# Performance work log

Measured on AMD Instinct MI355X. Metric: run time of the kernel, lower is better.

Reference implementation:

```python
import jax, jax.numpy as jnp
import numpy as np

B, NA, NT, P, DA, DM, H = 1, 4096, 1024, 32768, 128, 512, 4
DH = DA // H
DF = 4 * DA
WINDOW = 16


def _layer_norm(x, g=None, b=None, eps=1e-5):
    m = jnp.mean(x, axis=-1, keepdims=True)
    v = jnp.var(x, axis=-1, keepdims=True)
    xn = (x - m) / jnp.sqrt(v + eps)
    if g is not None:
        xn = xn * g + b
    return xn


def setup_inputs() -> dict:
    key = jax.random.key(0)
    ks = jax.random.split(key, 32)
    r = lambda k, s: (jax.random.normal(k, s, dtype=jnp.float32) * 0.05)
    return {
        'q': r(ks[0], (B, NA, DA)),
        'c_atom': r(ks[1], (B, NA, DA)),
        'h_cond': r(ks[2], (B, NT, DM)),
        'p_lm': r(ks[3], (B, P, 16)),
        't_emb': r(ks[4], (B, DA)),
        'cond_proj_w': r(ks[5], (DM, DA)), 'cond_proj_b': r(ks[6], (DA,)),
        'adaln1_w': r(ks[7], (DA, 2 * DA)), 'adaln1_b': r(ks[8], (2 * DA,)),
        'adaln2_w': r(ks[9], (DA, 2 * DA)), 'adaln2_b': r(ks[10], (2 * DA,)),
        'ln_g': jnp.ones((DA,), jnp.float32), 'ln_b': jnp.zeros((DA,), jnp.float32),
        'wq': r(ks[11], (DA, DA)), 'wk': r(ks[12], (DA, DA)),
        'wv': r(ks[13], (DA, DA)), 'wg': r(ks[14], (DA, DA)),
        'wo': r(ks[15], (DA, DA)),
        'pair_w': r(ks[16], (16, H)), 'pair_b': r(ks[17], (H,)),
        'gate1_w': r(ks[18], (DA, DA)), 'gate1_b': r(ks[19], (DA,)),
        'gate2_w': r(ks[20], (DA, DA)), 'gate2_b': r(ks[21], (DA,)),
        'sw1': r(ks[22], (DA, DF)), 'sw3': r(ks[23], (DA, DF)),
        'sw2': r(ks[24], (DF, DA)),
        'p_lm_idx': jax.random.randint(ks[25], (B, P, 2), 0, NA, dtype=jnp.int32),
        'token_idx': jnp.sort(jax.random.randint(ks[26], (B, NA), 0, NT, dtype=jnp.int32), axis=-1),
    }


def _forward(q, c_atom, h_cond, p_lm, t_emb,
             cond_proj_w, cond_proj_b, adaln1_w, adaln1_b, adaln2_w, adaln2_b,
             ln_g, ln_b, wq, wk, wv, wg, wo, pair_w, pair_b,
             gate1_w, gate1_b, gate2_w, gate2_b, sw1, sw3, sw2,
             p_lm_idx, token_idx):
    Bq, N, D = q.shape
    # gather token conditioning to atoms: (B, NA, DM)
    h_atoms = jax.vmap(lambda h, t: h[t])(h_cond, token_idx)
    cond = t_emb[:, None, :] + h_atoms @ cond_proj_w + cond_proj_b  # (B, NA, DA)
    g1, b1 = jnp.split(cond @ adaln1_w + adaln1_b, 2, axis=-1)
    q_n = (1.0 + g1) * _layer_norm(q, ln_g, ln_b) + b1

    Q = (q_n @ wq).reshape(Bq, N, H, DH)
    K = (q_n @ wk).reshape(Bq, N, H, DH)
    V = (q_n @ wv).reshape(Bq, N, H, DH)
    G_flat = q_n @ wg  # (B, N, DA); permute/reshape in torch is identity on layout

    scores = jnp.einsum('bihd,bjhd->bhij', Q, K) / jnp.sqrt(jnp.float32(DH))

    # scattered pair bias: (B, P, H) -> dense (B, H, N, N)
    bias = p_lm @ pair_w + pair_b  # (B, P, H)

    def scat(idx, bb):
        return jnp.zeros((N, N, H), bb.dtype).at[idx[:, 0], idx[:, 1]].set(bb)

    pair_bias = jax.vmap(scat)(p_lm_idx, bias).transpose(0, 3, 1, 2)
    scores = scores + pair_bias

    pos = jnp.arange(N)
    window = jnp.abs(pos[:, None] - pos[None, :]) <= WINDOW  # (N, N)
    scores = jnp.where(window[None, None, :, :], scores, -jnp.inf)

    attn = jax.nn.softmax(scores, axis=-1)
    att_out = jnp.einsum('bhij,bjhd->bihd', attn, V).reshape(Bq, N, D)

    q1 = q + jax.nn.sigmoid(G_flat) * (att_out @ wo)
    q1 = q1 + jax.nn.sigmoid(c_atom @ gate1_w + gate1_b) * q1

    g2, b2 = jnp.split(cond @ adaln2_w + adaln2_b, 2, axis=-1)
    q_n2 = (1.0 + g2) * _layer_norm(q1) + b2
    swi = (jax.nn.silu(q_n2 @ sw1) * (q_n2 @ sw3)) @ sw2
    q2 = q1 + jax.nn.sigmoid(c_atom @ gate2_w + gate2_b) * swi
    return q2  # atom_pad_mask is all-ones -> final mask multiply is identity


def reference(q, c_atom, h_cond, p_lm, t_emb,
              cond_proj_w, cond_proj_b, adaln1_w, adaln1_b, adaln2_w, adaln2_b,
              ln_g, ln_b, wq, wk, wv, wg, wo, pair_w, pair_b,
              gate1_w, gate1_b, gate2_w, gate2_b, sw1, sw3, sw2,
              p_lm_idx, token_idx):
    return _forward(q, c_atom, h_cond, p_lm, t_emb,
                    cond_proj_w, cond_proj_b, adaln1_w, adaln1_b, adaln2_w, adaln2_b,
                    ln_g, ln_b, wq, wk, wv, wg, wo, pair_w, pair_b,
                    gate1_w, gate1_b, gate2_w, gate2_b, sw1, sw3, sw2,
                    p_lm_idx, token_idx)
```

## Files before the change

### kernel.cpp

```cpp
#include <hip/hip_runtime.h>
#include <math.h>

#define NA   4096
#define DA   128
#define DM   512
#define NT   1024
#define HH   4
#define DF   512
#define PP   32768
#define WIN  16
#define BAND 33

typedef __attribute__((ext_vector_type(8))) short bf16x8;
typedef __attribute__((ext_vector_type(4))) float f32x4;

__device__ __forceinline__ float sigmoidf_(float x) { return 1.0f / (1.0f + __expf(-x)); }
__device__ __forceinline__ ushort f2bf(float f) {
    union { float f; unsigned int i; } x; x.f = f;
    unsigned int r = x.i + 0x7fffu + ((x.i >> 16) & 1u);
    return (ushort)(r >> 16);
}

__global__ __launch_bounds__(256) void k_prep(
    const float* __restrict__ hc, const float* __restrict__ ca,
    const float* __restrict__ cw, const float* __restrict__ a1, const float* __restrict__ a2,
    const float* __restrict__ wq, const float* __restrict__ wk, const float* __restrict__ wv,
    const float* __restrict__ wg, const float* __restrict__ wo,
    const float* __restrict__ g1, const float* __restrict__ g2,
    const float* __restrict__ s1, const float* __restrict__ s3, const float* __restrict__ s2,
    ushort* hcb, ushort* cab, ushort* cwT, ushort* a1T, ushort* a2T,
    ushort* wqT, ushort* wkT, ushort* wvT, ushort* wgT, ushort* woT,
    ushort* g1T, ushort* g2T, ushort* s1T, ushort* s3T, ushort* s2T)
{
    const float* src; ushort* dst; int logK = 0, N = 0, total = 0, tr = 1;
    switch (blockIdx.y) {
        case 0:  src = hc; dst = hcb; total = NT * DM; tr = 0; break;
        case 1:  src = ca; dst = cab; total = NA * DA; tr = 0; break;
        case 2:  src = cw; dst = cwT; logK = 9; N = 128; break;
        case 3:  src = a1; dst = a1T; logK = 7; N = 256; break;
        case 4:  src = a2; dst = a2T; logK = 7; N = 256; break;
        case 5:  src = wq; dst = wqT; logK = 7; N = 128; break;
        case 6:  src = wk; dst = wkT; logK = 7; N = 128; break;
        case 7:  src = wv; dst = wvT; logK = 7; N = 128; break;
        case 8:  src = wg; dst = wgT; logK = 7; N = 128; break;
        case 9:  src = wo; dst = woT; logK = 7; N = 128; break;
        case 10: src = g1; dst = g1T; logK = 7; N = 128; break;
        case 11: src = g2; dst = g2T; logK = 7; N = 128; break;
        case 12: src = s1; dst = s1T; logK = 7; N = 512; break;
        case 13: src = s3; dst = s3T; logK = 7; N = 512; break;
        default: src = s2; dst = s2T; logK = 9; N = 128; break;
    }
    if (tr) total = N << logK;
    for (int e = blockIdx.x * 256 + threadIdx.x; e < total; e += 64 * 256) {
        float v;
        if (tr) {
            int n = e >> logK, k = e & ((1 << logK) - 1);
            v = src[(size_t)k * N + n];
        } else {
            v = src[e];
        }
        dst[e] = f2bf(v);
    }
}

__global__ __launch_bounds__(256) void k_scatter(
    const float* __restrict__ p_lm, const float* __restrict__ pair_w,
    const float* __restrict__ pair_b, const int* __restrict__ idx,
    float* __restrict__ band)
{
    int p = blockIdx.x * 256 + threadIdx.x;
    if (p >= PP) return;
    int i = idx[2 * p], j = idx[2 * p + 1];
    int d = j - i + WIN;
    if (d < 0 || d > 2 * WIN) return;
    float v0 = pair_b[0], v1 = pair_b[1], v2 = pair_b[2], v3 = pair_b[3];
    #pragma unroll
    for (int k = 0; k < 16; ++k) {
        float a = p_lm[p * 16 + k];
        v0 = fmaf(a, pair_w[k * 4 + 0], v0);
        v1 = fmaf(a, pair_w[k * 4 + 1], v1);
        v2 = fmaf(a, pair_w[k * 4 + 2], v2);
        v3 = fmaf(a, pair_w[k * 4 + 3], v3);
    }
    size_t base = ((size_t)i * HH) * BAND + d;
    band[base + 0 * BAND] = v0;
    band[base + 1 * BAND] = v1;
    band[base + 2 * BAND] = v2;
    band[base + 3 * BAND] = v3;
}

template<int K, int NF>
__device__ __forceinline__ void gemm_core(
    const ushort* __restrict__ Arow, const ushort* __restrict__ WTcol,
    f32x4* acc, int ko)
{
    #pragma unroll
    for (int ks = 0; ks < K / 32; ++ks) {
        bf16x8 a = *(const bf16x8*)(Arow + ks * 32 + ko);
        #pragma unroll
        for (int nf = 0; nf < NF; ++nf) {
            bf16x8 b = *(const bf16x8*)(WTcol + (size_t)nf * 16 * K + ks * 32 + ko);
            acc[nf] = __builtin_amdgcn_mfma_f32_16x16x32_bf16(a, b, acc[nf], 0, 0, 0);
        }
    }
}

__global__ __launch_bounds__(256) void k_cond(
    const ushort* __restrict__ hcb, const int* __restrict__ tok,
    const ushort* __restrict__ cwT, const float* __restrict__ t_emb,
    const float* __restrict__ cond_b, ushort* __restrict__ cond_bf)
{
    const int tid = threadIdx.x, l = tid & 63, w = tid >> 6;
    const int cl = l & 15, ko = (l >> 4) * 8;
    const int m0 = blockIdx.x * 64, n0 = blockIdx.y * 32;
    const int trow = tok[m0 + w * 16 + cl];
    f32x4 acc[2] = {};
    gemm_core<512, 2>(hcb + (size_t)trow * DM, cwT + (size_t)(n0 + cl) * DM, acc, ko);
    const int r0 = m0 + w * 16 + (l >> 4) * 4;
    #pragma unroll
    for (int nf = 0; nf < 2; ++nf) {
        int col = n0 + nf * 16 + cl;
        float add = t_emb[col] + cond_b[col];
        #pragma unroll
        for (int r = 0; r < 4; ++r)
            cond_bf[(size_t)(r0 + r) * DA + col] = f2bf(acc[nf][r] + add);
    }
}

__global__ __launch_bounds__(256) void k_ada(
    const ushort* __restrict__ cond_bf,
    const ushort* __restrict__ a1T, const ushort* __restrict__ a2T,
    const float* __restrict__ b1, const float* __restrict__ b2,
    float* __restrict__ gb1, float* __restrict__ gb2)
{
    const int tid = threadIdx.x, l = tid & 63, w = tid >> 6;
    const int cl = l & 15, ko = (l >> 4) * 8;
    const int m0 = blockIdx.x * 64, n0 = blockIdx.y * 64;
    const ushort* WT = blockIdx.z ? a2T : a1T;
    const float* bias = blockIdx.z ? b2 : b1;
    float* O = blockIdx.z ? gb2 : gb1;
    f32x4 acc[4] = {};
    gemm_core<128, 4>(cond_bf + (size_t)(m0 + w * 16 + cl) * DA,
                      WT + (size_t)(n0 + cl) * DA, acc, ko);
    const int r0 = m0 + w * 16 + (l >> 4) * 4;
    #pragma unroll
    for (int nf = 0; nf < 4; ++nf) {
        int col = n0 + nf * 16 + cl;
        float bb = bias[col];
        #pragma unroll
        for (int r = 0; r < 4; ++r)
            O[(size_t)(r0 + r) * 256 + col] = acc[nf][r] + bb;
    }
}

__global__ __launch_bounds__(256) void k_gate(
    const ushort* __restrict__ cab,
    const ushort* __restrict__ g1T, const ushort* __restrict__ g2T,
    const float* __restrict__ b1, const float* __restrict__ b2,
    float* __restrict__ gate1, float* __restrict__ gate2)
{
    const int tid = threadIdx.x, l = tid & 63, w = tid >> 6;
    const int cl = l & 15, ko = (l >> 4) * 8;
    const int m0 = blockIdx.x * 64, n0 = blockIdx.y * 64;
    const ushort* WT = blockIdx.z ? g2T : g1T;
    const float* bias = blockIdx.z ? b2 : b1;
    float* O = blockIdx.z ? gate2 : gate1;
    f32x4 acc[4] = {};
    gemm_core<128, 4>(cab + (size_t)(m0 + w * 16 + cl) * DA,
                      WT + (size_t)(n0 + cl) * DA, acc, ko);
    const int r0 = m0 + w * 16 + (l >> 4) * 4;
    #pragma unroll
    for (int nf = 0; nf < 4; ++nf) {
        int col = n0 + nf * 16 + cl;
        float bb = bias[col];
        #pragma unroll
        for (int r = 0; r < 4; ++r)
            O[(size_t)(r0 + r) * DA + col] = sigmoidf_(acc[nf][r] + bb);
    }
}

template<int AFFINE>
__global__ __launch_bounds__(256) void k_ln(
    const float* __restrict__ x, const float* __restrict__ gb,
    const float* __restrict__ ln_g, const float* __restrict__ ln_b,
    ushort* __restrict__ out_bf)
{
    const int w = threadIdx.x >> 6, l = threadIdx.x & 63;
    const int row = blockIdx.x * 4 + w;
    float2 xv = *(const float2*)&x[(size_t)row * DA + 2 * l];
    float sum = xv.x + xv.y, sq = xv.x * xv.x + xv.y * xv.y;
    #pragma unroll
    for (int off = 1; off <= 32; off <<= 1) {
        sum += __shfl_xor(sum, off);
        sq  += __shfl_xor(sq,  off);
    }
    float m = sum * (1.0f / DA);
    float var = sq * (1.0f / DA) - m * m;
    float rs = rsqrtf(var + 1e-5f);
    float2 g = *(const float2*)&gb[(size_t)row * 256 + 2 * l];
    float2 b = *(const float2*)&gb[(size_t)row * 256 + 128 + 2 * l];
    float xn0 = (xv.x - m) * rs, xn1 = (xv.y - m) * rs;
    if (AFFINE) {
        float2 lg = *(const float2*)&ln_g[2 * l];
        float2 lb = *(const float2*)&ln_b[2 * l];
        xn0 = xn0 * lg.x + lb.x;
        xn1 = xn1 * lg.y + lb.y;
    }
    ushort2 st;
    st.x = f2bf((1.f + g.x) * xn0 + b.x);
    st.y = f2bf((1.f + g.y) * xn1 + b.y);
    *(ushort2*)&out_bf[(size_t)row * DA + 2 * l] = st;
}

__global__ __launch_bounds__(256) void k_qkvg(
    const ushort* __restrict__ qn_bf,
    const ushort* __restrict__ wqT, const ushort* __restrict__ wkT,
    const ushort* __restrict__ wvT, const ushort* __restrict__ wgT,
    float* __restrict__ Qb, float* __restrict__ Kb,
    float* __restrict__ Vb, float* __restrict__ sG)
{
    const int tid = threadIdx.x, l = tid & 63, w = tid >> 6;
    const int cl = l & 15, ko = (l >> 4) * 8;
    const int m0 = blockIdx.x * 64, n0 = blockIdx.y * 64;
    const int z = blockIdx.z;
    const ushort* WT = (z == 0) ? wqT : (z == 1) ? wkT : (z == 2) ? wvT : wgT;
    float* O = (z == 0) ? Qb : (z == 1) ? Kb : (z == 2) ? Vb : sG;
    f32x4 acc[4] = {};
    gemm_core<128, 4>(qn_bf + (size_t)(m0 + w * 16 + cl) * DA,
                      WT + (size_t)(n0 + cl) * DA, acc, ko);
    const int r0 = m0 + w * 16 + (l >> 4) * 4;
    #pragma unroll
    for (int nf = 0; nf < 4; ++nf) {
        int col = n0 + nf * 16 + cl;
        #pragma unroll
        for (int r = 0; r < 4; ++r) {
            float v = acc[nf][r];
            if (z == 3) v = sigmoidf_(v);
            O[(size_t)(r0 + r) * DA + col] = v;
        }
    }
}

__global__ __launch_bounds__(256) void k_attn(
    const float* __restrict__ Qb, const float* __restrict__ Kb,
    const float* __restrict__ Vb, const float* __restrict__ band,
    ushort* __restrict__ att_bf)
{
    const int tid = threadIdx.x;
    const int g = tid >> 3, l = tid & 7;
    const int i = blockIdx.x * 8 + (g >> 2), h = g & 3;
    const float scale = 0.17677669529663687f;
    float4 qr = *(const float4*)(Qb + (size_t)i * DA + h * 32 + l * 4);
    const float* brow = band + ((size_t)i * HH + h) * BAND;

    float s[BAND];
    float m = -1e30f;
    #pragma unroll
    for (int jo = 0; jo < BAND; ++jo) {
        int j = i - WIN + jo;
        float sv = -1e30f;
        if ((unsigned)j < NA) {
            float4 kk = *(const float4*)(Kb + (size_t)j * DA + h * 32 + l * 4);
            float d = 0.f;
            d = fmaf(qr.x, kk.x, d); d = fmaf(qr.y, kk.y, d);
            d = fmaf(qr.z, kk.z, d); d = fmaf(qr.w, kk.w, d);
            d += __shfl_xor(d, 1);
            d += __shfl_xor(d, 2);
            d += __shfl_xor(d, 4);
            sv = fmaf(d, scale, brow[jo]);
        }
        s[jo] = sv;
        m = fmaxf(m, sv);
    }
    float lsum = 0.f;
    #pragma unroll
    for (int jo = 0; jo < BAND; ++jo) {
        float p = __expf(s[jo] - m);
        s[jo] = p;
        lsum += p;
    }
    float inv = 1.0f / lsum;
    float4 o = {0.f, 0.f, 0.f, 0.f};
    #pragma unroll
    for (int jo = 0; jo < BAND; ++jo) {
        int j = i - WIN + jo;
        if ((unsigned)j < NA) {
            float4 v = *(const float4*)(Vb + (size_t)j * DA + h * 32 + l * 4);
            o.x = fmaf(s[jo], v.x, o.x);
            o.y = fmaf(s[jo], v.y, o.y);
            o.z = fmaf(s[jo], v.z, o.z);
            o.w = fmaf(s[jo], v.w, o.w);
        }
    }
    ushort4 st;
    st.x = f2bf(o.x * inv); st.y = f2bf(o.y * inv);
    st.z = f2bf(o.z * inv); st.w = f2bf(o.w * inv);
    *(ushort4*)&att_bf[(size_t)i * DA + h * 32 + l * 4] = st;
}

__global__ __launch_bounds__(256) void k_wo(
    const ushort* __restrict__ att_bf, const ushort* __restrict__ woT,
    const float* __restrict__ q, const float* __restrict__ sG,
    const float* __restrict__ gate1, float* __restrict__ q1)
{
    const int tid = threadIdx.x, l = tid & 63, w = tid >> 6;
    const int cl = l & 15, ko = (l >> 4) * 8;
    const int m0 = blockIdx.x * 64, n0 = blockIdx.y * 32;
    f32x4 acc[2] = {};
    gemm_core<128, 2>(att_bf + (size_t)(m0 + w * 16 + cl) * DA,
                      woT + (size_t)(n0 + cl) * DA, acc, ko);
    const int r0 = m0 + w * 16 + (l >> 4) * 4;
    #pragma unroll
    for (int nf = 0; nf < 2; ++nf) {
        int col = n0 + nf * 16 + cl;
        #pragma unroll
        for (int r = 0; r < 4; ++r) {
            size_t rc = (size_t)(r0 + r) * DA + col;
            q1[rc] = (q[rc] + sG[rc] * acc[nf][r]) * (1.f + gate1[rc]);
        }
    }
}

__global__ __launch_bounds__(256) void k_sw13(
    const ushort* __restrict__ qn2_bf,
    const ushort* __restrict__ s1T, const ushort* __restrict__ s3T,
    ushort* __restrict__ hb_bf)
{
    const int tid = threadIdx.x, l = tid & 63, w = tid >> 6;
    const int cl = l & 15, ko = (l >> 4) * 8;
    const int m0 = blockIdx.x * 64, n0 = blockIdx.y * 64;
    const ushort* Arow = qn2_bf + (size_t)(m0 + w * 16 + cl) * DA;
    const ushort* W1 = s1T + (size_t)(n0 + cl) * DA;
    const ushort* W3 = s3T + (size_t)(n0 + cl) * DA;
    f32x4 acc1[4] = {}, acc3[4] = {};
    #pragma unroll
    for (int ks = 0; ks < 4; ++ks) {
        bf16x8 a = *(const bf16x8*)(Arow + ks * 32 + ko);
        #pragma unroll
        for (int nf = 0; nf < 4; ++nf) {
            bf16x8 b1 = *(const bf16x8*)(W1 + (size_t)nf * 16 * DA + ks * 32 + ko);
            acc1[nf] = __builtin_amdgcn_mfma_f32_16x16x32_bf16(a, b1, acc1[nf], 0, 0, 0);
            bf16x8 b3 = *(const bf16x8*)(W3 + (size_t)nf * 16 * DA + ks * 32 + ko);
            acc3[nf] = __builtin_amdgcn_mfma_f32_16x16x32_bf16(a, b3, acc3[nf], 0, 0, 0);
        }
    }
    const int r0 = m0 + w * 16 + (l >> 4) * 4;
    #pragma unroll
    for (int nf = 0; nf < 4; ++nf) {
        int col = n0 + nf * 16 + cl;
        #pragma unroll
        for (int r = 0; r < 4; ++r) {
            float x1 = acc1[nf][r], x3 = acc3[nf][r];
            hb_bf[(size_t)(r0 + r) * DF + col] = f2bf(x1 * sigmoidf_(x1) * x3);
        }
    }
}

__global__ __launch_bounds__(256) void k_sw2(
    const ushort* __restrict__ hb_bf, const ushort* __restrict__ s2T,
    const float* __restrict__ q1, const float* __restrict__ gate2,
    float* __restrict__ out)
{
    const int tid = threadIdx.x, l = tid & 63, w = tid >> 6;
    const int cl = l & 15, ko = (l >> 4) * 8;
    const int m0 = blockIdx.x * 64, n0 = blockIdx.y * 32;
    f32x4 acc[2] = {};
    gemm_core<512, 2>(hb_bf + (size_t)(m0 + w * 16 + cl) * DF,
                      s2T + (size_t)(n0 + cl) * DF, acc, ko);
    const int r0 = m0 + w * 16 + (l >> 4) * 4;
    #pragma unroll
    for (int nf = 0; nf < 2; ++nf) {
        int col = n0 + nf * 16 + cl;
        #pragma unroll
        for (int r = 0; r < 4; ++r) {
            size_t rc = (size_t)(r0 + r) * DA + col;
            out[rc] = q1[rc] + gate2[rc] * acc[nf][r];
        }
    }
}

extern "C" void kernel_launch(void* const* d_in, const int* in_sizes, int n_in,
                              void* d_out, int out_size, void* d_ws, size_t ws_size,
                              hipStream_t stream)
{
    const float* q      = (const float*)d_in[0];
    const float* c_atom = (const float*)d_in[1];
    const float* h_cond = (const float*)d_in[2];
    const float* p_lm   = (const float*)d_in[3];
    const float* t_emb  = (const float*)d_in[4];
    const float* cond_w = (const float*)d_in[5];
    const float* cond_b = (const float*)d_in[6];
    const float* ad1w   = (const float*)d_in[7];
    const float* ad1b   = (const float*)d_in[8];
    const float* ad2w   = (const float*)d_in[9];
    const float* ad2b   = (const float*)d_in[10];
    const float* ln_g   = (const float*)d_in[11];
    const float* ln_b   = (const float*)d_in[12];
    const float* wq     = (const float*)d_in[13];
    const float* wk     = (const float*)d_in[14];
    const float* wv     = (const float*)d_in[15];
    const float* wg     = (const float*)d_in[16];
    const float* wo     = (const float*)d_in[17];
    const float* pair_w = (const float*)d_in[18];
    const float* pair_b = (const float*)d_in[19];
    const float* g1w    = (const float*)d_in[20];
    const float* g1b    = (const float*)d_in[21];
    const float* g2w    = (const float*)d_in[22];
    const float* g2b    = (const float*)d_in[23];
    const float* sw1    = (const float*)d_in[24];
    const float* sw3    = (const float*)d_in[25];
    const float* sw2    = (const float*)d_in[26];
    const int*   p_idx  = (const int*)d_in[27];
    const int*   tok    = (const int*)d_in[28];
    float* out = (float*)d_out;

    size_t off = 0;
    char* base = (char*)d_ws;
    auto alloc = [&](size_t bytes) -> void* {
        void* p = base + off;
        off += (bytes + 255) & ~(size_t)255;
        return p;
    };
    ushort* hcb     = (ushort*)alloc((size_t)NT * DM * 2);
    ushort* cab     = (ushort*)alloc((size_t)NA * DA * 2);
    ushort* cwT     = (ushort*)alloc((size_t)DM * DA * 2);
    ushort* a1T     = (ushort*)alloc((size_t)256 * 128 * 2);
    ushort* a2T     = (ushort*)alloc((size_t)256 * 128 * 2);
    ushort* wqT     = (ushort*)alloc((size_t)128 * 128 * 2);
    ushort* wkT     = (ushort*)alloc((size_t)128 * 128 * 2);
    ushort* wvT     = (ushort*)alloc((size_t)128 * 128 * 2);
    ushort* wgT     = (ushort*)alloc((size_t)128 * 128 * 2);
    ushort* woT     = (ushort*)alloc((size_t)128 * 128 * 2);
    ushort* g1T     = (ushort*)alloc((size_t)128 * 128 * 2);
    ushort* g2T     = (ushort*)alloc((size_t)128 * 128 * 2);
    ushort* s1T     = (ushort*)alloc((size_t)512 * 128 * 2);
    ushort* s3T     = (ushort*)alloc((size_t)512 * 128 * 2);
    ushort* s2T     = (ushort*)alloc((size_t)128 * 512 * 2);
    ushort* cond_bf = (ushort*)alloc((size_t)NA * DA * 2);
    float*  gb1     = (float*)alloc((size_t)NA * 256 * 4);
    float*  gb2     = (float*)alloc((size_t)NA * 256 * 4);
    float*  gate1   = (float*)alloc((size_t)NA * DA * 4);
    float*  gate2   = (float*)alloc((size_t)NA * DA * 4);
    ushort* qn_bf   = (ushort*)alloc((size_t)NA * DA * 2);
    float*  Qb      = (float*)alloc((size_t)NA * DA * 4);
    float*  Kb      = (float*)alloc((size_t)NA * DA * 4);
    float*  Vb      = (float*)alloc((size_t)NA * DA * 4);
    float*  sG      = (float*)alloc((size_t)NA * DA * 4);
    float*  band    = (float*)alloc((size_t)NA * HH * BAND * 4);
    ushort* att_bf  = (ushort*)alloc((size_t)NA * DA * 2);
    float*  q1      = (float*)alloc((size_t)NA * DA * 4);
    ushort* qn2_bf  = (ushort*)alloc((size_t)NA * DA * 2);
    ushort* hb_bf   = (ushort*)alloc((size_t)NA * DF * 2);

    k_prep<<<dim3(64, 15), 256, 0, stream>>>(
        h_cond, c_atom, cond_w, ad1w, ad2w, wq, wk, wv, wg, wo,
        g1w, g2w, sw1, sw3, sw2,
        hcb, cab, cwT, a1T, a2T, wqT, wkT, wvT, wgT, woT,
        g1T, g2T, s1T, s3T, s2T);
    hipMemsetAsync(band, 0, (size_t)NA * HH * BAND * sizeof(float), stream);
    k_scatter<<<PP / 256, 256, 0, stream>>>(p_lm, pair_w, pair_b, p_idx, band);
    k_cond<<<dim3(64, 4), 256, 0, stream>>>(hcb, tok, cwT, t_emb, cond_b, cond_bf);
    k_ada<<<dim3(64, 4, 2), 256, 0, stream>>>(cond_bf, a1T, a2T, ad1b, ad2b, gb1, gb2);
    k_gate<<<dim3(64, 2, 2), 256, 0, stream>>>(cab, g1T, g2T, g1b, g2b, gate1, gate2);
    k_ln<1><<<NA / 4, 256, 0, stream>>>(q, gb1, ln_g, ln_b, qn_bf);
    k_qkvg<<<dim3(64, 2, 4), 256, 0, stream>>>(qn_bf, wqT, wkT, wvT, wgT, Qb, Kb, Vb, sG);
    k_attn<<<NA / 8, 256, 0, stream>>>(Qb, Kb, Vb, band, att_bf);
    k_wo<<<dim3(64, 4), 256, 0, stream>>>(att_bf, woT, q, sG, gate1, q1);
    k_ln<0><<<NA / 4, 256, 0, stream>>>(q1, gb2, ln_g, ln_b, qn2_bf);
    k_sw13<<<dim3(64, 8), 256, 0, stream>>>(qn2_bf, s1T, s3T, hb_bf);
    k_sw2<<<dim3(64, 4), 256, 0, stream>>>(hb_bf, s2T, q1, gate2, out);
    (void)in_sizes; (void)n_in; (void)out_size; (void)ws_size;
}
```

Baseline: 206.5 us.

## Fuse pipeline into fewer kernels: LN into GEMMs, attn+wo, full FFN

Collapses the launch sequence from about twelve launches to six. Band and output zeroing move into the prep kernel, which now uses tiled shared-memory transposes. The pair scatter is folded into the cond kernel, and the adaLN and gate GEMMs are merged into one launch. Layer norm is computed inside the QKVG and FFN kernels, attention is fused with the Wo projection, and the SwiGLU FFN keeps its hidden tile in swizzled LDS with split-K atomicAdd into a zeroed output. This removes intermediate global buffers and launch gaps, but adds atomics and redundant LN recomputation across the column blocks.

```diff
diff --git a/kernel.cpp b/kernel.cpp
--- a/kernel.cpp
+++ b/kernel.cpp
@@ -21,6 +21,22 @@
     return (ushort)(r >> 16);
 }
 
+template<int K, int NF>
+__device__ __forceinline__ void gemm_core(
+    const ushort* __restrict__ Arow, const ushort* __restrict__ WTcol,
+    f32x4* acc, int ko)
+{
+    #pragma unroll
+    for (int ks = 0; ks < K / 32; ++ks) {
+        bf16x8 a = *(const bf16x8*)(Arow + ks * 32 + ko);
+        #pragma unroll
+        for (int nf = 0; nf < NF; ++nf) {
+            bf16x8 b = *(const bf16x8*)(WTcol + (size_t)nf * 16 * K + ks * 32 + ko);
+            acc[nf] = __builtin_amdgcn_mfma_f32_16x16x32_bf16(a, b, acc[nf], 0, 0, 0);
+        }
+    }
+}
+
 __global__ __launch_bounds__(256) void k_prep(
     const float* __restrict__ hc, const float* __restrict__ ca,
     const float* __restrict__ cw, const float* __restrict__ a1, const float* __restrict__ a2,
@@ -30,89 +46,102 @@
     const float* __restrict__ s1, const float* __restrict__ s3, const float* __restrict__ s2,
     ushort* hcb, ushort* cab, ushort* cwT, ushort* a1T, ushort* a2T,
     ushort* wqT, ushort* wkT, ushort* wvT, ushort* wgT, ushort* woT,
-    ushort* g1T, ushort* g2T, ushort* s1T, ushort* s3T, ushort* s2T)
-{
-    const float* src; ushort* dst; int logK = 0, N = 0, total = 0, tr = 1;
-    switch (blockIdx.y) {
-        case 0:  src = hc; dst = hcb; total = NT * DM; tr = 0; break;
-        case 1:  src = ca; dst = cab; total = NA * DA; tr = 0; break;
-        case 2:  src = cw; dst = cwT; logK = 9; N = 128; break;
-        case 3:  src = a1; dst = a1T; logK = 7; N = 256; break;
-        case 4:  src = a2; dst = a2T; logK = 7; N = 256; break;
-        case 5:  src = wq; dst = wqT; logK = 7; N = 128; break;
-        case 6:  src = wk; dst = wkT; logK = 7; N = 128; break;
-        case 7:  src = wv; dst = wvT; logK = 7; N = 128; break;
-        case 8:  src = wg; dst = wgT; logK = 7; N = 128; break;
-        case 9:  src = wo; dst = woT; logK = 7; N = 128; break;
-        case 10: src = g1; dst = g1T; logK = 7; N = 128; break;
-        case 11: src = g2; dst = g2T; logK = 7; N = 128; break;
-        case 12: src = s1; dst = s1T; logK = 7; N = 512; break;
-        case 13: src = s3; dst = s3T; logK = 7; N = 512; break;
-        default: src = s2; dst = s2T; logK = 9; N = 128; break;
-    }
-    if (tr) total = N << logK;
-    for (int e = blockIdx.x * 256 + threadIdx.x; e < total; e += 64 * 256) {
-        float v;
-        if (tr) {
-            int n = e >> logK, k = e & ((1 << logK) - 1);
-            v = src[(size_t)k * N + n];
-        } else {
-            v = src[e];
-        }
-        dst[e] = f2bf(v);
-    }
-}
-
-__global__ __launch_bounds__(256) void k_scatter(
-    const float* __restrict__ p_lm, const float* __restrict__ pair_w,
-    const float* __restrict__ pair_b, const int* __restrict__ idx,
-    float* __restrict__ band)
-{
-    int p = blockIdx.x * 256 + threadIdx.x;
-    if (p >= PP) return;
-    int i = idx[2 * p], j = idx[2 * p + 1];
-    int d = j - i + WIN;
-    if (d < 0 || d > 2 * WIN) return;
-    float v0 = pair_b[0], v1 = pair_b[1], v2 = pair_b[2], v3 = pair_b[3];
-    #pragma unroll
-    for (int k = 0; k < 16; ++k) {
-        float a = p_lm[p * 16 + k];
-        v0 = fmaf(a, pair_w[k * 4 + 0], v0);
-        v1 = fmaf(a, pair_w[k * 4 + 1], v1);
-        v2 = fmaf(a, pair_w[k * 4 + 2], v2);
-        v3 = fmaf(a, pair_w[k * 4 + 3], v3);
-    }
-    size_t base = ((size_t)i * HH) * BAND + d;
-    band[base + 0 * BAND] = v0;
-    band[base + 1 * BAND] = v1;
-    band[base + 2 * BAND] = v2;
-    band[base + 3 * BAND] = v3;
-}
-
-template<int K, int NF>
-__device__ __forceinline__ void gemm_core(
-    const ushort* __restrict__ Arow, const ushort* __restrict__ WTcol,
-    f32x4* acc, int ko)
-{
-    #pragma unroll
-    for (int ks = 0; ks < K / 32; ++ks) {
-        bf16x8 a = *(const bf16x8*)(Arow + ks * 32 + ko);
-        #pragma unroll
-        for (int nf = 0; nf < NF; ++nf) {
-            bf16x8 b = *(const bf16x8*)(WTcol + (size_t)nf * 16 * K + ks * 32 + ko);
-            acc[nf] = __builtin_amdgcn_mfma_f32_16x16x32_bf16(a, b, acc[nf], 0, 0, 0);
-        }
+    ushort* g1T, ushort* g2T, ushort* s1T, ushort* s3T, ushort* s2T,
+    float* band, float* outz)
+{
+    __shared__ float tile[32][33];
+    const int y = blockIdx.y, bx = blockIdx.x, tid = threadIdx.x;
+    if (y <= 1) {
+        const float4* src = (const float4*)(y == 0 ? hc : ca);
+        ushort* dst = y == 0 ? hcb : cab;
+        for (int i = bx * 256 + tid; i < 131072; i += 16384) {
+            float4 v = src[i];
+            ushort4 st; st.x = f2bf(v.x); st.y = f2bf(v.y); st.z = f2bf(v.z); st.w = f2bf(v.w);
+            *(ushort4*)&dst[(size_t)i * 4] = st;
+        }
+        return;
+    }
+    if (y == 15) {
+        float4 z = {0.f, 0.f, 0.f, 0.f};
+        float4* b4 = (float4*)band;
+        for (int i = bx * 256 + tid; i < 135168; i += 16384) b4[i] = z;
+        return;
+    }
+    if (y == 16) {
+        float4 z = {0.f, 0.f, 0.f, 0.f};
+        float4* o4 = (float4*)outz;
+        for (int i = bx * 256 + tid; i < 131072; i += 16384) o4[i] = z;
+        return;
+    }
+    const float* src; ushort* dst; int K, N;
+    switch (y) {
+        case 2:  src = cw; dst = cwT; K = 512; N = 128; break;
+        case 3:  src = a1; dst = a1T; K = 128; N = 256; break;
+        case 4:  src = a2; dst = a2T; K = 128; N = 256; break;
+        case 5:  src = wq; dst = wqT; K = 128; N = 128; break;
+        case 6:  src = wk; dst = wkT; K = 128; N = 128; break;
+        case 7:  src = wv; dst = wvT; K = 128; N = 128; break;
+        case 8:  src = wg; dst = wgT; K = 128; N = 128; break;
+        case 9:  src = wo; dst = woT; K = 128; N = 128; break;
+        case 10: src = g1; dst = g1T; K = 128; N = 128; break;
+        case 11: src = g2; dst = g2T; K = 128; N = 128; break;
+        case 12: src = s1; dst = s1T; K = 128; N = 512; break;
+        case 13: src = s3; dst = s3T; K = 128; N = 512; break;
+        default: src = s2; dst = s2T; K = 512; N = 128; break;
+    }
+    const int tn_cnt = N >> 5;
+    if (bx >= (K >> 5) * tn_cnt) return;
+    const int k0 = (bx / tn_cnt) << 5, n0 = (bx % tn_cnt) << 5;
+    {
+        int r = tid >> 3, c = (tid & 7) << 2;
+        float4 v = *(const float4*)&src[(size_t)(k0 + r) * N + n0 + c];
+        tile[r][c + 0] = v.x; tile[r][c + 1] = v.y;
+        tile[r][c + 2] = v.z; tile[r][c + 3] = v.w;
+    }
+    __syncthreads();
+    {
+        int rn = tid >> 3, ck = (tid & 7) << 2;
+        ushort4 st;
+        st.x = f2bf(tile[ck + 0][rn]);
+        st.y = f2bf(tile[ck + 1][rn]);
+        st.z = f2bf(tile[ck + 2][rn]);
+        st.w = f2bf(tile[ck + 3][rn]);
+        *(ushort4*)&dst[(size_t)(n0 + rn) * K + k0 + ck] = st;
     }
 }
 
 __global__ __launch_bounds__(256) void k_cond(
     const ushort* __restrict__ hcb, const int* __restrict__ tok,
     const ushort* __restrict__ cwT, const float* __restrict__ t_emb,
-    const float* __restrict__ cond_b, ushort* __restrict__ cond_bf)
-{
-    const int tid = threadIdx.x, l = tid & 63, w = tid >> 6;
-    const int cl = l & 15, ko = (l >> 4) * 8;
-    const int m0 = blockIdx.x * 64, n0 = blockIdx.y * 32;
+    const float* __restrict__ cond_b, ushort* __restrict__ cond_bf,
+    const float* __restrict__ p_lm, const float* __restrict__ pair_w,
+    const float* __restrict__ pair_b, const int* __restrict__ p_idx,
+    float* __restrict__ band)
+{
+    const int tid = threadIdx.x, y = blockIdx.y;
+    if (y >= 4) {
+        int p = ((y - 4) * 64 + blockIdx.x) * 256 + tid;
+        int i = p_idx[2 * p], j = p_idx[2 * p + 1];
+        int d = j - i + WIN;
+        if (d < 0 || d > 2 * WIN) return;
+        float v0 = pair_b[0], v1 = pair_b[1], v2 = pair_b[2], v3 = pair_b[3];
+        #pragma unroll
+        for (int k = 0; k < 16; ++k) {
+            float a = p_lm[p * 16 + k];
+            v0 = fmaf(a, pair_w[k * 4 + 0], v0);
+            v1 = fmaf(a, pair_w[k * 4 + 1], v1);
+            v2 = fmaf(a, pair_w[k * 4 + 2], v2);
+            v3 = fmaf(a, pair_w[k * 4 + 3], v3);
+        }
+        size_t base = ((size_t)i * HH) * BAND + d;
+        band[base + 0 * BAND] = v0;
+        band[base + 1 * BAND] = v1;
+        band[base + 2 * BAND] = v2;
+        band[base + 3 * BAND] = v3;
+        return;
+    }
+    const int l = tid & 63, w = tid >> 6, cl = l & 15, ko = (l >> 4) * 8;
+    const int m0 = blockIdx.x * 64, n0 = y * 32;
     const int trow = tok[m0 + w * 16 + cl];
     f32x4 acc[2] = {};
     gemm_core<512, 2>(hcb + (size_t)trow * DM, cwT + (size_t)(n0 + cl) * DM, acc, ko);
@@ -127,108 +156,104 @@
     }
 }
 
-__global__ __launch_bounds__(256) void k_ada(
-    const ushort* __restrict__ cond_bf,
+__global__ __launch_bounds__(256) void k_modgate(
+    const ushort* __restrict__ cond_bf, const ushort* __restrict__ cab,
     const ushort* __restrict__ a1T, const ushort* __restrict__ a2T,
-    const float* __restrict__ b1, const float* __restrict__ b2,
-    float* __restrict__ gb1, float* __restrict__ gb2)
-{
-    const int tid = threadIdx.x, l = tid & 63, w = tid >> 6;
-    const int cl = l & 15, ko = (l >> 4) * 8;
-    const int m0 = blockIdx.x * 64, n0 = blockIdx.y * 64;
-    const ushort* WT = blockIdx.z ? a2T : a1T;
-    const float* bias = blockIdx.z ? b2 : b1;
-    float* O = blockIdx.z ? gb2 : gb1;
+    const ushort* __restrict__ g1T, const ushort* __restrict__ g2T,
+    const float* __restrict__ ad1b, const float* __restrict__ ad2b,
+    const float* __restrict__ g1b, const float* __restrict__ g2b,
+    float* __restrict__ gb1, float* __restrict__ gb2,
+    float* __restrict__ gate1, float* __restrict__ gate2)
+{
+    const int tid = threadIdx.x, y = blockIdx.y;
+    const int l = tid & 63, w = tid >> 6, cl = l & 15, ko = (l >> 4) * 8;
+    const int m0 = blockIdx.x * 64;
+    const ushort* A; const ushort* WT; const float* bias; float* O; int ldo, n0, sig;
+    if (y < 4)       { A = cond_bf; WT = a1T; bias = ad1b; O = gb1;   ldo = 256; n0 = y * 64;        sig = 0; }
+    else if (y < 8)  { A = cond_bf; WT = a2T; bias = ad2b; O = gb2;   ldo = 256; n0 = (y - 4) * 64;  sig = 0; }
+    else if (y < 10) { A = cab;     WT = g1T; bias = g1b;  O = gate1; ldo = 128; n0 = (y - 8) * 64;  sig = 1; }
+    else             { A = cab;     WT = g2T; bias = g2b;  O = gate2; ldo = 128; n0 = (y - 10) * 64; sig = 1; }
     f32x4 acc[4] = {};
-    gemm_core<128, 4>(cond_bf + (size_t)(m0 + w * 16 + cl) * DA,
-                      WT + (size_t)(n0 + cl) * DA, acc, ko);
+    gemm_core<128, 4>(A + (size_t)(m0 + w * 16 + cl) * DA, WT + (size_t)(n0 + cl) * DA, acc, ko);
     const int r0 = m0 + w * 16 + (l >> 4) * 4;
     #pragma unroll
     for (int nf = 0; nf < 4; ++nf) {
         int col = n0 + nf * 16 + cl;
         float bb = bias[col];
         #pragma unroll
-        for (int r = 0; r < 4; ++r)
-            O[(size_t)(r0 + r) * 256 + col] = acc[nf][r] + bb;
-    }
-}
-
-__global__ __launch_bounds__(256) void k_gate(
-    const ushort* __restrict__ cab,
-    const ushort* __restrict__ g1T, const ushort* __restrict__ g2T,
-    const float* __restrict__ b1, const float* __restrict__ b2,
-    float* __restrict__ gate1, float* __restrict__ gate2)
-{
-    const int tid = threadIdx.x, l = tid & 63, w = tid >> 6;
-    const int cl = l & 15, ko = (l >> 4) * 8;
-    const int m0 = blockIdx.x * 64, n0 = blockIdx.y * 64;
-    const ushort* WT = blockIdx.z ? g2T : g1T;
-    const float* bias = blockIdx.z ? b2 : b1;
-    float* O = blockIdx.z ? gate2 : gate1;
-    f32x4 acc[4] = {};
-    gemm_core<128, 4>(cab + (size_t)(m0 + w * 16 + cl) * DA,
-                      WT + (size_t)(n0 + cl) * DA, acc, ko);
-    const int r0 = m0 + w * 16 + (l >> 4) * 4;
-    #pragma unroll
-    for (int nf = 0; nf < 4; ++nf) {
-        int col = n0 + nf * 16 + cl;
-        float bb = bias[col];
-        #pragma unroll
-        for (int r = 0; r < 4; ++r)
-            O[(size_t)(r0 + r) * DA + col] = sigmoidf_(acc[nf][r] + bb);
-    }
-}
-
-template<int AFFINE>
-__global__ __launch_bounds__(256) void k_ln(
-    const float* __restrict__ x, const float* __restrict__ gb,
+        for (int r = 0; r < 4; ++r) {
+            float v = acc[nf][r] + bb;
+            if (sig) v = sigmoidf_(v);
+            O[(size_t)(r0 + r) * ldo + col] = v;
+        }
+    }
+}
+
+__global__ __launch_bounds__(256) void k_qkvg(
+    const float* __restrict__ q, const float* __restrict__ gb1,
     const float* __restrict__ ln_g, const float* __restrict__ ln_b,
-    ushort* __restrict__ out_bf)
-{
-    const int w = threadIdx.x >> 6, l = threadIdx.x & 63;
-    const int row = blockIdx.x * 4 + w;
-    float2 xv = *(const float2*)&x[(size_t)row * DA + 2 * l];
-    float sum = xv.x + xv.y, sq = xv.x * xv.x + xv.y * xv.y;
-    #pragma unroll
-    for (int off = 1; off <= 32; off <<= 1) {
-        sum += __shfl_xor(sum, off);
-        sq  += __shfl_xor(sq,  off);
-    }
-    float m = sum * (1.0f / DA);
-    float var = sq * (1.0f / DA) - m * m;
-    float rs = rsqrtf(var + 1e-5f);
-    float2 g = *(const float2*)&gb[(size_t)row * 256 + 2 * l];
-    float2 b = *(const float2*)&gb[(size_t)row * 256 + 128 + 2 * l];
-    float xn0 = (xv.x - m) * rs, xn1 = (xv.y - m) * rs;
-    if (AFFINE) {
-        float2 lg = *(const float2*)&ln_g[2 * l];
-        float2 lb = *(const float2*)&ln_b[2 * l];
-        xn0 = xn0 * lg.x + lb.x;
-        xn1 = xn1 * lg.y + lb.y;
-    }
-    ushort2 st;
-    st.x = f2bf((1.f + g.x) * xn0 + b.x);
-    st.y = f2bf((1.f + g.y) * xn1 + b.y);
-    *(ushort2*)&out_bf[(size_t)row * DA + 2 * l] = st;
-}
-
-__global__ __launch_bounds__(256) void k_qkvg(
-    const ushort* __restrict__ qn_bf,
     const ushort* __restrict__ wqT, const ushort* __restrict__ wkT,
     const ushort* __restrict__ wvT, const ushort* __restrict__ wgT,
     float* __restrict__ Qb, float* __restrict__ Kb,
     float* __restrict__ Vb, float* __restrict__ sG)
 {
     const int tid = threadIdx.x, l = tid & 63, w = tid >> 6;
-    const int cl = l & 15, ko = (l >> 4) * 8;
-    const int m0 = blockIdx.x * 64, n0 = blockIdx.y * 64;
-    const int z = blockIdx.z;
+    const int cl = l & 15, kq = l >> 4, ko = kq * 8;
+    const int m0 = blockIdx.x * 64, n0 = blockIdx.y * 64, z = blockIdx.z;
+    const int row = m0 + w * 16 + cl;
+
+    float qv[4][8];
+    float sum = 0.f, sq = 0.f;
+    #pragma unroll
+    for (int ks = 0; ks < 4; ++ks) {
+        float4 v0 = *(const float4*)&q[(size_t)row * DA + ks * 32 + ko];
+        float4 v1 = *(const float4*)&q[(size_t)row * DA + ks * 32 + ko + 4];
+        qv[ks][0] = v0.x; qv[ks][1] = v0.y; qv[ks][2] = v0.z; qv[ks][3] = v0.w;
+        qv[ks][4] = v1.x; qv[ks][5] = v1.y; qv[ks][6] = v1.z; qv[ks][7] = v1.w;
+        sum += v0.x + v0.y + v0.z + v0.w + v1.x + v1.y + v1.z + v1.w;
+        sq += v0.x * v0.x + v0.y * v0.y + v0.z * v0.z + v0.w * v0.w
+            + v1.x * v1.x + v1.y * v1.y + v1.z * v1.z + v1.w * v1.w;
+    }
+    sum += __shfl_xor(sum, 16); sq += __shfl_xor(sq, 16);
+    sum += __shfl_xor(sum, 32); sq += __shfl_xor(sq, 32);
+    float mean = sum * (1.0f / DA);
+    float rs = rsqrtf(sq * (1.0f / DA) - mean * mean + 1e-5f);
+
+    bf16x8 afr[4];
+    #pragma unroll
+    for (int ks = 0; ks < 4; ++ks) {
+        int k = ks * 32 + ko;
+        float4 lg0 = *(const float4*)&ln_g[k], lg1 = *(const float4*)&ln_g[k + 4];
+        float4 lb0 = *(const float4*)&ln_b[k], lb1 = *(const float4*)&ln_b[k + 4];
+        float4 g0 = *(const float4*)&gb1[(size_t)row * 256 + k];
+        float4 g1v = *(const float4*)&gb1[(size_t)row * 256 + k + 4];
+        float4 b0 = *(const float4*)&gb1[(size_t)row * 256 + 128 + k];
+        float4 b1v = *(const float4*)&gb1[(size_t)row * 256 + 128 + k + 4];
+        float lg[8] = {lg0.x, lg0.y, lg0.z, lg0.w, lg1.x, lg1.y, lg1.z, lg1.w};
+        float lb[8] = {lb0.x, lb0.y, lb0.z, lb0.w, lb1.x, lb1.y, lb1.z, lb1.w};
+        float gg[8] = {g0.x, g0.y, g0.z, g0.w, g1v.x, g1v.y, g1v.z, g1v.w};
+        float bb[8] = {b0.x, b0.y, b0.z, b0.w, b1v.x, b1v.y, b1v.z, b1v.w};
+        #pragma unroll
+        for (int j = 0; j < 8; ++j) {
+            float xn = (qv[ks][j] - mean) * rs;
+            float yv = (1.f + gg[j]) * (xn * lg[j] + lb[j]) + bb[j];
+            afr[ks][j] = (short)f2bf(yv);
+        }
+    }
+
     const ushort* WT = (z == 0) ? wqT : (z == 1) ? wkT : (z == 2) ? wvT : wgT;
     float* O = (z == 0) ? Qb : (z == 1) ? Kb : (z == 2) ? Vb : sG;
+    const ushort* Wc = WT + (size_t)(n0 + cl) * DA;
     f32x4 acc[4] = {};
-    gemm_core<128, 4>(qn_bf + (size_t)(m0 + w * 16 + cl) * DA,
-                      WT + (size_t)(n0 + cl) * DA, acc, ko);
-    const int r0 = m0 + w * 16 + (l >> 4) * 4;
+    #pragma unroll
+    for (int ks = 0; ks < 4; ++ks) {
+        #pragma unroll
+        for (int nf = 0; nf < 4; ++nf) {
+            bf16x8 b = *(const bf16x8*)(Wc + (size_t)nf * 16 * DA + ks * 32 + ko);
+            acc[nf] = __builtin_amdgcn_mfma_f32_16x16x32_bf16(afr[ks], b, acc[nf], 0, 0, 0);
+        }
+    }
+    const int r0 = m0 + w * 16 + kq * 4;
     #pragma unroll
     for (int nf = 0; nf < 4; ++nf) {
         int col = n0 + nf * 16 + cl;
@@ -241,140 +266,192 @@
     }
 }
 
-__global__ __launch_bounds__(256) void k_attn(
+__global__ __launch_bounds__(512) void k_attnwo(
     const float* __restrict__ Qb, const float* __restrict__ Kb,
     const float* __restrict__ Vb, const float* __restrict__ band,
-    ushort* __restrict__ att_bf)
-{
+    const float* __restrict__ q, const float* __restrict__ sG,
+    const float* __restrict__ gate1, const ushort* __restrict__ woT,
+    float* __restrict__ q1)
+{
+    __shared__ ushort att_s[16 * 128];
     const int tid = threadIdx.x;
-    const int g = tid >> 3, l = tid & 7;
-    const int i = blockIdx.x * 8 + (g >> 2), h = g & 3;
-    const float scale = 0.17677669529663687f;
-    float4 qr = *(const float4*)(Qb + (size_t)i * DA + h * 32 + l * 4);
-    const float* brow = band + ((size_t)i * HH + h) * BAND;
-
-    float s[BAND];
-    float m = -1e30f;
-    #pragma unroll
-    for (int jo = 0; jo < BAND; ++jo) {
-        int j = i - WIN + jo;
-        float sv = -1e30f;
-        if ((unsigned)j < NA) {
-            float4 kk = *(const float4*)(Kb + (size_t)j * DA + h * 32 + l * 4);
-            float d = 0.f;
-            d = fmaf(qr.x, kk.x, d); d = fmaf(qr.y, kk.y, d);
-            d = fmaf(qr.z, kk.z, d); d = fmaf(qr.w, kk.w, d);
-            d += __shfl_xor(d, 1);
-            d += __shfl_xor(d, 2);
-            d += __shfl_xor(d, 4);
-            sv = fmaf(d, scale, brow[jo]);
-        }
-        s[jo] = sv;
-        m = fmaxf(m, sv);
-    }
-    float lsum = 0.f;
-    #pragma unroll
-    for (int jo = 0; jo < BAND; ++jo) {
-        float p = __expf(s[jo] - m);
-        s[jo] = p;
-        lsum += p;
-    }
-    float inv = 1.0f / lsum;
-    float4 o = {0.f, 0.f, 0.f, 0.f};
-    #pragma unroll
-    for (int jo = 0; jo < BAND; ++jo) {
-        int j = i - WIN + jo;
-        if ((unsigned)j < NA) {
-            float4 v = *(const float4*)(Vb + (size_t)j * DA + h * 32 + l * 4);
-            o.x = fmaf(s[jo], v.x, o.x);
-            o.y = fmaf(s[jo], v.y, o.y);
-            o.z = fmaf(s[jo], v.z, o.z);
-            o.w = fmaf(s[jo], v.w, o.w);
-        }
-    }
-    ushort4 st;
-    st.x = f2bf(o.x * inv); st.y = f2bf(o.y * inv);
-    st.z = f2bf(o.z * inv); st.w = f2bf(o.w * inv);
-    *(ushort4*)&att_bf[(size_t)i * DA + h * 32 + l * 4] = st;
-}
-
-__global__ __launch_bounds__(256) void k_wo(
-    const ushort* __restrict__ att_bf, const ushort* __restrict__ woT,
-    const float* __restrict__ q, const float* __restrict__ sG,
-    const float* __restrict__ gate1, float* __restrict__ q1)
-{
+    const int r0 = blockIdx.x * 16;
+    {
+        const int g = tid >> 3, l3 = tid & 7;
+        const int rl = g >> 2, h = g & 3;
+        const int i = r0 + rl;
+        const float scale = 0.17677669529663687f;
+        float4 qr = *(const float4*)(Qb + (size_t)i * DA + h * 32 + l3 * 4);
+        const float* brow = band + ((size_t)i * HH + h) * BAND;
+        float s[BAND];
+        float m = -1e30f;
+        #pragma unroll
+        for (int jo = 0; jo < BAND; ++jo) {
+            int j = i - WIN + jo;
+            float sv = -1e30f;
+            if ((unsigned)j < NA) {
+                float4 kk = *(const float4*)(Kb + (size_t)j * DA + h * 32 + l3 * 4);
+                float d = 0.f;
+                d = fmaf(qr.x, kk.x, d); d = fmaf(qr.y, kk.y, d);
+                d = fmaf(qr.z, kk.z, d); d = fmaf(qr.w, kk.w, d);
+                d += __shfl_xor(d, 1);
+                d += __shfl_xor(d, 2);
+                d += __shfl_xor(d, 4);
+                sv = fmaf(d, scale, brow[jo]);
+            }
+            s[jo] = sv;
+            m = fmaxf(m, sv);
+        }
+        float lsum = 0.f;
+        #pragma unroll
+        for (int jo = 0; jo < BAND; ++jo) {
+            float p = __expf(s[jo] - m);
+            s[jo] = p;
+            lsum += p;
+        }
+        float inv = 1.0f / lsum;
+        float4 o = {0.f, 0.f, 0.f, 0.f};
+        #pragma unroll
+        for (int jo = 0; jo < BAND; ++jo) {
+            int j = i - WIN + jo;
+            if ((unsigned)j < NA) {
+                float4 v = *(const float4*)(Vb + (size_t)j * DA + h * 32 + l3 * 4);
+                o.x = fmaf(s[jo], v.x, o.x);
+                o.y = fmaf(s[jo], v.y, o.y);
+                o.z = fmaf(s[jo], v.z, o.z);
+                o.w = fmaf(s[jo], v.w, o.w);
+            }
+        }
+        ushort4 st;
+        st.x = f2bf(o.x * inv); st.y = f2bf(o.y * inv);
+        st.z = f2bf(o.z * inv); st.w = f2bf(o.w * inv);
+        int byte = rl * 256 + h * 64 + l3 * 8;
+        byte ^= (rl & 7) << 4;
+        *(ushort4*)((char*)att_s + byte) = st;
+    }
+    __syncthreads();
+    {
+        const int l = tid & 63, w = tid >> 6;
+        const int cl = l & 15, kq = l >> 4, ko = kq * 8;
+        const int n0 = w * 16;
+        f32x4 acc = {0.f, 0.f, 0.f, 0.f};
+        #pragma unroll
+        for (int ks = 0; ks < 4; ++ks) {
+            int byteA = cl * 256 + (ks * 32 + ko) * 2;
+            byteA ^= (cl & 7) << 4;
+            bf16x8 a = *(const bf16x8*)((char*)att_s + byteA);
+            bf16x8 b = *(const bf16x8*)(woT + (size_t)(n0 + cl) * DA + ks * 32 + ko);
+            acc = __builtin_amdgcn_mfma_f32_16x16x32_bf16(a, b, acc, 0, 0, 0);
+        }
+        #pragma unroll
+        for (int r = 0; r < 4; ++r) {
+            int row = r0 + kq * 4 + r, col = n0 + cl;
+            size_t rc = (size_t)row * DA + col;
+            q1[rc] = (q[rc] + sG[rc] * acc[r]) * (1.f + gate1[rc]);
+        }
+    }
+}
+
+__global__ __launch_bounds__(256) void k_ffn(
+    const float* __restrict__ q1, const float* __restrict__ gb2,
+    const float* __restrict__ gate2,
+    const ushort* __restrict__ s1T, const ushort* __restrict__ s3T,
+    const ushort* __restrict__ s2T, float* __restrict__ out)
+{
+    __shared__ ushort hbs[16 * 128];
     const int tid = threadIdx.x, l = tid & 63, w = tid >> 6;
-    const int cl = l & 15, ko = (l >> 4) * 8;
-    const int m0 = blockIdx.x * 64, n0 = blockIdx.y * 32;
-    f32x4 acc[2] = {};
-    gemm_core<128, 2>(att_bf + (size_t)(m0 + w * 16 + cl) * DA,
-                      woT + (size_t)(n0 + cl) * DA, acc, ko);
-    const int r0 = m0 + w * 16 + (l >> 4) * 4;
-    #pragma unroll
-    for (int nf = 0; nf < 2; ++nf) {
-        int col = n0 + nf * 16 + cl;
-        #pragma unroll
-        for (int r = 0; r < 4; ++r) {
-            size_t rc = (size_t)(r0 + r) * DA + col;
-            q1[rc] = (q[rc] + sG[rc] * acc[nf][r]) * (1.f + gate1[rc]);
-        }
-    }
-}
-
-__global__ __launch_bounds__(256) void k_sw13(
-    const ushort* __restrict__ qn2_bf,
-    const ushort* __restrict__ s1T, const ushort* __restrict__ s3T,
-    ushort* __restrict__ hb_bf)
-{
-    const int tid = threadIdx.x, l = tid & 63, w = tid >> 6;
-    const int cl = l & 15, ko = (l >> 4) * 8;
-    const int m0 = blockIdx.x * 64, n0 = blockIdx.y * 64;
-    const ushort* Arow = qn2_bf + (size_t)(m0 + w * 16 + cl) * DA;
-    const ushort* W1 = s1T + (size_t)(n0 + cl) * DA;
-    const ushort* W3 = s3T + (size_t)(n0 + cl) * DA;
-    f32x4 acc1[4] = {}, acc3[4] = {};
+    const int cl = l & 15, kq = l >> 4, ko = kq * 8;
+    const int m0 = blockIdx.x * 16;
+    const int by = blockIdx.y;
+    const int row = m0 + cl;
+
+    float qv[4][8];
+    float sum = 0.f, sq = 0.f;
     #pragma unroll
     for (int ks = 0; ks < 4; ++ks) {
-        bf16x8 a = *(const bf16x8*)(Arow + ks * 32 + ko);
-        #pragma unroll
-        for (int nf = 0; nf < 4; ++nf) {
-            bf16x8 b1 = *(const bf16x8*)(W1 + (size_t)nf * 16 * DA + ks * 32 + ko);
-            acc1[nf] = __builtin_amdgcn_mfma_f32_16x16x32_bf16(a, b1, acc1[nf], 0, 0, 0);
-            bf16x8 b3 = *(const bf16x8*)(W3 + (size_t)nf * 16 * DA + ks * 32 + ko);
-            acc3[nf] = __builtin_amdgcn_mfma_f32_16x16x32_bf16(a, b3, acc3[nf], 0, 0, 0);
-        }
-    }
-    const int r0 = m0 + w * 16 + (l >> 4) * 4;
-    #pragma unroll
-    for (int nf = 0; nf < 4; ++nf) {
-        int col = n0 + nf * 16 + cl;
-        #pragma unroll
-        for (int r = 0; r < 4; ++r) {
-            float x1 = acc1[nf][r], x3 = acc3[nf][r];
-            hb_bf[(size_t)(r0 + r) * DF + col] = f2bf(x1 * sigmoidf_(x1) * x3);
-        }
-    }
-}
-
-__global__ __launch_bounds__(256) void k_sw2(
-    const ushort* __restrict__ hb_bf, const ushort* __restrict__ s2T,
-    const float* __restrict__ q1, const float* __restrict__ gate2,
-    float* __restrict__ out)
-{
-    const int tid = threadIdx.x, l = tid & 63, w = tid >> 6;
-    const int cl = l & 15, ko = (l >> 4) * 8;
-    const int m0 = blockIdx.x * 64, n0 = blockIdx.y * 32;
-    f32x4 acc[2] = {};
-    gemm_core<512, 2>(hb_bf + (size_t)(m0 + w * 16 + cl) * DF,
-                      s2T + (size_t)(n0 + cl) * DF, acc, ko);
-    const int r0 = m0 + w * 16 + (l >> 4) * 4;
-    #pragma unroll
-    for (int nf = 0; nf < 2; ++nf) {
-        int col = n0 + nf * 16 + cl;
-        #pragma unroll
-        for (int r = 0; r < 4; ++r) {
-            size_t rc = (size_t)(r0 + r) * DA + col;
-            out[rc] = q1[rc] + gate2[rc] * acc[nf][r];
+        float4 v0 = *(const float4*)&q1[(size_t)row * DA + ks * 32 + ko];
+        float4 v1 = *(const float4*)&q1[(size_t)row * DA + ks * 32 + ko + 4];
+        qv[ks][0] = v0.x; qv[ks][1] = v0.y; qv[ks][2] = v0.z; qv[ks][3] = v0.w;
+        qv[ks][4] = v1.x; qv[ks][5] = v1.y; qv[ks][6] = v1.z; qv[ks][7] = v1.w;
+        sum += v0.x + v0.y + v0.z + v0.w + v1.x + v1.y + v1.z + v1.w;
+        sq += v0.x * v0.x + v0.y * v0.y + v0.z * v0.z + v0.w * v0.w
+            + v1.x * v1.x + v1.y * v1.y + v1.z * v1.z + v1.w * v1.w;
+    }
+    sum += __shfl_xor(sum, 16); sq += __shfl_xor(sq, 16);
+    sum += __shfl_xor(sum, 32); sq += __shfl_xor(sq, 32);
+    float mean = sum * (1.0f / DA);
+    float rs = rsqrtf(sq * (1.0f / DA) - mean * mean + 1e-5f);
+
+    bf16x8 afr[4];
+    #pragma unroll
+    for (int ks = 0; ks < 4; ++ks) {
+        int k = ks * 32 + ko;
+        float4 g0 = *(const float4*)&gb2[(size_t)row * 256 + k];
+        float4 g1v = *(const float4*)&gb2[(size_t)row * 256 + k + 4];
+        float4 b0 = *(const float4*)&gb2[(size_t)row * 256 + 128 + k];
+        float4 b1v = *(const float4*)&gb2[(size_t)row * 256 + 128 + k + 4];
+        float gg[8] = {g0.x, g0.y, g0.z, g0.w, g1v.x, g1v.y, g1v.z, g1v.w};
+        float bb[8] = {b0.x, b0.y, b0.z, b0.w, b1v.x, b1v.y, b1v.z, b1v.w};
+        #pragma unroll
+        for (int j = 0; j < 8; ++j) {
+            float xn = (qv[ks][j] - mean) * rs;
+            afr[ks][j] = (short)f2bf((1.f + gg[j]) * xn + bb[j]);
+        }
+    }
+
+    {
+        const ushort* W1 = s1T + (size_t)(by * 128 + w * 32 + cl) * DA;
+        const ushort* W3 = s3T + (size_t)(by * 128 + w * 32 + cl) * DA;
+        f32x4 acc1[2] = {}, acc3[2] = {};
+        #pragma unroll
+        for (int ks = 0; ks < 4; ++ks) {
+            #pragma unroll
+            for (int nf = 0; nf < 2; ++nf) {
+                bf16x8 b1 = *(const bf16x8*)(W1 + (size_t)nf * 16 * DA + ks * 32 + ko);
+                acc1[nf] = __builtin_amdgcn_mfma_f32_16x16x32_bf16(afr[ks], b1, acc1[nf], 0, 0, 0);
+                bf16x8 b3 = *(const bf16x8*)(W3 + (size_t)nf * 16 * DA + ks * 32 + ko);
+                acc3[nf] = __builtin_amdgcn_mfma_f32_16x16x32_bf16(afr[ks], b3, acc3[nf], 0, 0, 0);
+            }
+        }
+        #pragma unroll
+        for (int nf = 0; nf < 2; ++nf) {
+            #pragma unroll
+            for (int r = 0; r < 4; ++r) {
+                float x1 = acc1[nf][r], x3 = acc3[nf][r];
+                float h = x1 * sigmoidf_(x1) * x3;
+                int rr = kq * 4 + r;
+                int col = w * 32 + nf * 16 + cl;
+                int byte = rr * 256 + col * 2;
+                byte ^= (rr & 7) << 4;
+                *(ushort*)((char*)hbs + byte) = f2bf(h);
+            }
+        }
+    }
+    __syncthreads();
+    {
+        const ushort* W2 = s2T + (size_t)(w * 32 + cl) * DF + by * 128;
+        f32x4 acc[2] = {};
+        #pragma unroll
+        for (int ks = 0; ks < 4; ++ks) {
+            int byteA = cl * 256 + (ks * 32 + ko) * 2;
+            byteA ^= (cl & 7) << 4;
+            bf16x8 a = *(const bf16x8*)((char*)hbs + byteA);
+            #pragma unroll
+            for (int nf = 0; nf < 2; ++nf) {
+                bf16x8 b = *(const bf16x8*)(W2 + (size_t)nf * 16 * DF + ks * 32 + ko);
+                acc[nf] = __builtin_amdgcn_mfma_f32_16x16x32_bf16(a, b, acc[nf], 0, 0, 0);
+            }
+        }
+        #pragma unroll
+        for (int nf = 0; nf < 2; ++nf) {
+            #pragma unroll
+            for (int r = 0; r < 4; ++r) {
+                int rowg = m0 + kq * 4 + r, col = w * 32 + nf * 16 + cl;
+                size_t rc = (size_t)rowg * DA + col;
+                float val = gate2[rc] * acc[nf][r];
+                if (by == 0) val += q1[rc];
+                atomicAdd(&out[rc], val);
+            }
         }
     }
 }
@@ -441,33 +518,26 @@
     float*  gb2     = (float*)alloc((size_t)NA * 256 * 4);
     float*  gate1   = (float*)alloc((size_t)NA * DA * 4);
     float*  gate2   = (float*)alloc((size_t)NA * DA * 4);
-    ushort* qn_bf   = (ushort*)alloc((size_t)NA * DA * 2);
     float*  Qb      = (float*)alloc((size_t)NA * DA * 4);
     float*  Kb      = (float*)alloc((size_t)NA * DA * 4);
     float*  Vb      = (float*)alloc((size_t)NA * DA * 4);
     float*  sG      = (float*)alloc((size_t)NA * DA * 4);
     float*  band    = (float*)alloc((size_t)NA * HH * BAND * 4);
-    ushort* att_bf  = (ushort*)alloc((size_t)NA * DA * 2);
     float*  q1      = (float*)alloc((size_t)NA * DA * 4);
-    ushort* qn2_bf  = (ushort*)alloc((size_t)NA * DA * 2);
-    ushort* hb_bf   = (ushort*)alloc((size_t)NA * DF * 2);
-
-    k_prep<<<dim3(64, 15), 256, 0, stream>>>(
+
+    k_prep<<<dim3(64, 17), 256, 0, stream>>>(
         h_cond, c_atom, cond_w, ad1w, ad2w, wq, wk, wv, wg, wo,
         g1w, g2w, sw1, sw3, sw2,
         hcb, cab, cwT, a1T, a2T, wqT, wkT, wvT, wgT, woT,
-        g1T, g2T, s1T, s3T, s2T);
-    hipMemsetAsync(band, 0, (size_t)NA * HH * BAND * sizeof(float), stream);
-    k_scatter<<<PP / 256, 256, 0, stream>>>(p_lm, pair_w, pair_b, p_idx, band);
-    k_cond<<<dim3(64, 4), 256, 0, stream>>>(hcb, tok, cwT, t_emb, cond_b, cond_bf);
-    k_ada<<<dim3(64, 4, 2), 256, 0, stream>>>(cond_bf, a1T, a2T, ad1b, ad2b, gb1, gb2);
-    k_gate<<<dim3(64, 2, 2), 256, 0, stream>>>(cab, g1T, g2T, g1b, g2b, gate1, gate2);
-    k_ln<1><<<NA / 4, 256, 0, stream>>>(q, gb1, ln_g, ln_b, qn_bf);
-    k_qkvg<<<dim3(64, 2, 4), 256, 0, stream>>>(qn_bf, wqT, wkT, wvT, wgT, Qb, Kb, Vb, sG);
-    k_attn<<<NA / 8, 256, 0, stream>>>(Qb, Kb, Vb, band, att_bf);
-    k_wo<<<dim3(64, 4), 256, 0, stream>>>(att_bf, woT, q, sG, gate1, q1);
-    k_ln<0><<<NA / 4, 256, 0, stream>>>(q1, gb2, ln_g, ln_b, qn2_bf);
-    k_sw13<<<dim3(64, 8), 256, 0, stream>>>(qn2_bf, s1T, s3T, hb_bf);
-    k_sw2<<<dim3(64, 4), 256, 0, stream>>>(hb_bf, s2T, q1, gate2, out);
+        g1T, g2T, s1T, s3T, s2T, band, out);
+    k_cond<<<dim3(64, 6), 256, 0, stream>>>(hcb, tok, cwT, t_emb, cond_b, cond_bf,
+                                            p_lm, pair_w, pair_b, p_idx, band);
+    k_modgate<<<dim3(64, 12), 256, 0, stream>>>(cond_bf, cab, a1T, a2T, g1T, g2T,
+                                                ad1b, ad2b, g1b, g2b,
+                                                gb1, gb2, gate1, gate2);
+    k_qkvg<<<dim3(64, 2, 4), 256, 0, stream>>>(q, gb1, ln_g, ln_b,
+                                               wqT, wkT, wvT, wgT, Qb, Kb, Vb, sG);
+    k_attnwo<<<NA / 16, 512, 0, stream>>>(Qb, Kb, Vb, band, q, sG, gate1, woT, q1);
+    k_ffn<<<dim3(NA / 16, 4), 256, 0, stream>>>(q1, gb2, gate2, s1T, s3T, s2T, out);
     (void)in_sizes; (void)n_in; (void)out_size; (void)ws_size;
 }
```

After: 198.8 us. 3.7% less time.
